# Optimization experiments

Measured on AMD Instinct MI355X. Metric: run time of the kernel, lower is better.

The kernel has to match this reference:

```python
import jax, jax.numpy as jnp
import numpy as np

N_NODES = 40000
N_EDGES = 640000
IN_CH = 128
HID_CH = 128
BN_EPS = 1e-5


def setup_inputs() -> dict:
    key = jax.random.key(0)
    k_x, k_ei, k_w, k_g = jax.random.split(key, 4)
    x = jax.random.normal(k_x, (N_NODES, IN_CH), dtype=jnp.float32)
    edge_index = jax.random.randint(k_ei, (2, N_EDGES), 0, N_NODES, dtype=jnp.int32)
    # Glorot init for GCNConv weight, zero bias (PyG defaults)
    limit = float(np.sqrt(6.0 / (IN_CH + HID_CH)))
    W = jax.random.uniform(k_w, (IN_CH, HID_CH), dtype=jnp.float32, minval=-limit, maxval=limit)
    b = jnp.zeros((HID_CH,), dtype=jnp.float32)
    gamma = jnp.ones((HID_CH,), dtype=jnp.float32)
    beta = jnp.zeros((HID_CH,), dtype=jnp.float32)
    return {"x": x, "edge_index": edge_index, "W": W, "b": b, "gamma": gamma, "beta": beta}


def reference(x, edge_index, W, b, gamma, beta):
    N = x.shape[0]
    src, dst = edge_index[0], edge_index[1]

    # --- GCNConv: h = x @ W, symmetric-normalized aggregation with self-loops ---
    h = x @ W  # [N, H]
    ones = jnp.ones((src.shape[0],), dtype=x.dtype)
    deg = jax.ops.segment_sum(ones, dst, num_segments=N) + 1.0  # +1 for self-loop
    dinv = jax.lax.rsqrt(deg)  # deg >= 1 always
    norm = dinv[src] * dinv[dst]  # [E]
    msg = h[src] * norm[:, None]  # [E, H] gather
    agg = jax.ops.segment_sum(msg, dst, num_segments=N)  # scatter-add
    agg = agg + h * (dinv * dinv)[:, None]  # self-loop contribution
    out = agg + b  # bias added after aggregation (PyG GCNConv)

    # --- BatchNorm1d (training mode: batch stats, biased variance) ---
    mean = jnp.mean(out, axis=0)
    var = jnp.mean((out - mean) ** 2, axis=0)
    out = gamma * (out - mean) * jax.lax.rsqrt(var + BN_EPS) + beta

    # --- ReLU (dropout is a no-op in eval) ---
    return jax.nn.relu(out)
```

## Files before the change

kernel.cpp:

```cpp
#include <hip/hip_runtime.h>

#define N_NODES 40000
#define N_EDGES 640000
#define CH 128
#define BN_EPS 1e-5f
#define CAP 48
#define CNT_S 8
#define MM_ROWS 32
#define MM_BLOCKS (N_NODES / MM_ROWS)
#define FILL_BLOCKS (N_EDGES / 512)


typedef __bf16 bf16x8 __attribute__((ext_vector_type(8)));
typedef float f32x4 __attribute__((ext_vector_type(4)));

__device__ __forceinline__ float bf_lo(unsigned u) { return __uint_as_float(u << 16); }
__device__ __forceinline__ float bf_hi(unsigned u) { return __uint_as_float(u & 0xffff0000u); }
__device__ __forceinline__ unsigned short f2bf(float f) {
    unsigned u = __float_as_uint(f);
    unsigned r = 0x7fffu + ((u >> 16) & 1u);
    return (unsigned short)((u + r) >> 16);
}
__device__ __forceinline__ unsigned pack2bf(float a, float b) {
    return (unsigned)f2bf(a) | ((unsigned)f2bf(b) << 16);
}

__global__ __launch_bounds__(256) void mm_kernel(const float* __restrict__ x,
                                                 const float* __restrict__ W,
                                                 unsigned short* __restrict__ hbf) {
    __shared__ unsigned xl[MM_ROWS * 68];
    int t = threadIdx.x;
    int bb = blockIdx.x;
    size_t row0 = (size_t)bb * MM_ROWS;
#pragma unroll
    for (int it = 0; it < MM_ROWS * 32 / 256; ++it) {
        int idx = it * 256 + t;
        int row = idx >> 5, c4 = idx & 31;
        float4 f = ((const float4*)(x + (row0 + row) * CH))[c4];
        uint2 p;
        p.x = pack2bf(f.x, f.y);
        p.y = pack2bf(f.z, f.w);
        *(uint2*)&xl[row * 68 + 2 * c4] = p;
    }
    int w = t >> 6, l = t & 63;
    int q = l >> 4, c15 = l & 15;
    int ct0 = 2 * w, ct1 = 2 * w + 1;
    bf16x8 bf0[4], bf1[4];
#pragma unroll
    for (int ks = 0; ks < 4; ++ks) {
        const float* wp = W + (size_t)(ks * 32 + 8 * q) * CH + c15;
        float v0[8], v1[8];
#pragma unroll
        for (int j = 0; j < 8; ++j) {
            v0[j] = wp[j * CH + ct0 * 16];
            v1[j] = wp[j * CH + ct1 * 16];
        }
        uint4 u0, u1;
        u0.x = pack2bf(v0[0], v0[1]); u0.y = pack2bf(v0[2], v0[3]);
        u0.z = pack2bf(v0[4], v0[5]); u0.w = pack2bf(v0[6], v0[7]);
        u1.x = pack2bf(v1[0], v1[1]); u1.y = pack2bf(v1[2], v1[3]);
        u1.z = pack2bf(v1[4], v1[5]); u1.w = pack2bf(v1[6], v1[7]);
        bf0[ks] = __builtin_bit_cast(bf16x8, u0);
        bf1[ks] = __builtin_bit_cast(bf16x8, u1);
    }
    __syncthreads();
#pragma unroll
    for (int rt = 0; rt < MM_ROWS / 16; ++rt) {
        int rbase = rt * 16 + c15;
        f32x4 acc0 = {0.f, 0.f, 0.f, 0.f};
        f32x4 acc1 = {0.f, 0.f, 0.f, 0.f};
#pragma unroll
        for (int ks = 0; ks < 4; ++ks) {
            uint4 ua = *(const uint4*)&xl[rbase * 68 + ks * 16 + 4 * q];
            bf16x8 af = __builtin_bit_cast(bf16x8, ua);
            acc0 = __builtin_amdgcn_mfma_f32_16x16x32_bf16(af, bf0[ks], acc0, 0, 0, 0);
            acc1 = __builtin_amdgcn_mfma_f32_16x16x32_bf16(af, bf1[ks], acc1, 0, 0, 0);
        }
        unsigned short* hr = hbf + (row0 + rt * 16 + q * 4) * CH;
#pragma unroll
        for (int r = 0; r < 4; ++r) {
            hr[r * CH + ct0 * 16 + c15] = f2bf(acc0[r]);
            hr[r * CH + ct1 * 16 + c15] = f2bf(acc1[r]);
        }
    }
}

__global__ __launch_bounds__(256) void fill_kernel(const int* __restrict__ src,
                                                   const int* __restrict__ dst,
                                                   int* __restrict__ cnt,
                                                   unsigned short* __restrict__ bucket16) {
    int t = threadIdx.x;
    int bb = blockIdx.x;
    int base = cnt[N_NODES * CNT_S];
    int i0 = bb * 512 + t;
    int i1 = i0 + 256;
    int d0 = dst[i0], d1 = dst[i1];
    int s0 = src[i0], s1 = src[i1];
    int sl0 = atomicAdd(&cnt[d0 * CNT_S], 1) - base;
    int sl1 = atomicAdd(&cnt[d1 * CNT_S], 1) - base;
    if (sl0 < CAP) bucket16[d0 * CAP + sl0] = (unsigned short)s0;
    if (sl1 < CAP) bucket16[d1 * CAP + sl1] = (unsigned short)s1;
}

__global__ __launch_bounds__(256) void aggregate_kernel(const unsigned short* __restrict__ bucket16,
                                                        const int* __restrict__ cnt,
                                                        const unsigned short* __restrict__ hbf,
                                                        const float* __restrict__ b,
                                                        float* __restrict__ out,
                                                        float* __restrict__ sums32) {
    __shared__ float bsum[CH], bsq[CH];
    int t = threadIdx.x;
    if (t < CH) { bsum[t] = 0.0f; bsq[t] = 0.0f; }
    __syncthreads();
    int base = cnt[N_NODES * CNT_S];
    int wid = t >> 6;
    int lane = t & 63;
    int quarter = lane >> 4;
    int ql = lane & 15;
    const uint4* h4 = (const uint4*)hbf;
    float4 bv0 = ((const float4*)b)[ql * 2];
    float4 bv1 = ((const float4*)b)[ql * 2 + 1];
    int n_base = blockIdx.x * 16 + wid * 4;
    float s0 = 0, s1 = 0, s2 = 0, s3 = 0, s4 = 0, s5 = 0, s6 = 0, s7 = 0;
    float q0 = 0, q1 = 0, q2 = 0, q3 = 0, q4 = 0, q5 = 0, q6 = 0, q7 = 0;
#pragma unroll 1
    for (int it = 0; it < 4; ++it) {
        int n = n_base + it;
        int cn = cnt[n * CNT_S] - base;
        int m = cn < CAP ? cn : CAP;
        float dn = rsqrtf((float)cn + 1.0f);
        unsigned sx_pre = (lane < m) ? (unsigned)bucket16[n * CAP + lane] : 0u;
        float a0 = 0, a1 = 0, a2 = 0, a3 = 0, a4 = 0, a5 = 0, a6 = 0, a7 = 0;
        for (int jj = 0; jj < m; jj += 16) {
            int e = jj + quarter * 4;
            unsigned sx0 = (unsigned)__shfl((int)sx_pre, e, 64);
            unsigned sx1 = (unsigned)__shfl((int)sx_pre, e + 1, 64);
            unsigned sx2 = (unsigned)__shfl((int)sx_pre, e + 2, 64);
            unsigned sx3 = (unsigned)__shfl((int)sx_pre, e + 3, 64);
            int c0g = cnt[sx0 * CNT_S];
            int c1g = cnt[sx1 * CNT_S];
            int c2g = cnt[sx2 * CNT_S];
            int c3g = cnt[sx3 * CNT_S];
            uint4 r0 = h4[(size_t)sx0 * 16 + ql];
            uint4 r1 = h4[(size_t)sx1 * 16 + ql];
            uint4 r2 = h4[(size_t)sx2 * 16 + ql];
            uint4 r3 = h4[(size_t)sx3 * 16 + ql];
            float d0 = (e     < m) ? rsqrtf((float)(c0g - base) + 1.0f) : 0.0f;
            float d1 = (e + 1 < m) ? rsqrtf((float)(c1g - base) + 1.0f) : 0.0f;
            float d2 = (e + 2 < m) ? rsqrtf((float)(c2g - base) + 1.0f) : 0.0f;
            float d3 = (e + 3 < m) ? rsqrtf((float)(c3g - base) + 1.0f) : 0.0f;
            a0 += bf_lo(r0.x) * d0; a1 += bf_hi(r0.x) * d0;
            a2 += bf_lo(r0.y) * d0; a3 += bf_hi(r0.y) * d0;
            a4 += bf_lo(r0.z) * d0; a5 += bf_hi(r0.z) * d0;
            a6 += bf_lo(r0.w) * d0; a7 += bf_hi(r0.w) * d0;
            a0 += bf_lo(r1.x) * d1; a1 += bf_hi(r1.x) * d1;
            a2 += bf_lo(r1.y) * d1; a3 += bf_hi(r1.y) * d1;
            a4 += bf_lo(r1.z) * d1; a5 += bf_hi(r1.z) * d1;
            a6 += bf_lo(r1.w) * d1; a7 += bf_hi(r1.w) * d1;
            a0 += bf_lo(r2.x) * d2; a1 += bf_hi(r2.x) * d2;
            a2 += bf_lo(r2.y) * d2; a3 += bf_hi(r2.y) * d2;
            a4 += bf_lo(r2.z) * d2; a5 += bf_hi(r2.z) * d2;
            a6 += bf_lo(r2.w) * d2; a7 += bf_hi(r2.w) * d2;
            a0 += bf_lo(r3.x) * d3; a1 += bf_hi(r3.x) * d3;
            a2 += bf_lo(r3.y) * d3; a3 += bf_hi(r3.y) * d3;
            a4 += bf_lo(r3.z) * d3; a5 += bf_hi(r3.z) * d3;
            a6 += bf_lo(r3.w) * d3; a7 += bf_hi(r3.w) * d3;
        }
        a0 += __shfl_xor(a0, 16, 64); a0 += __shfl_xor(a0, 32, 64);
        a1 += __shfl_xor(a1, 16, 64); a1 += __shfl_xor(a1, 32, 64);
        a2 += __shfl_xor(a2, 16, 64); a2 += __shfl_xor(a2, 32, 64);
        a3 += __shfl_xor(a3, 16, 64); a3 += __shfl_xor(a3, 32, 64);
        a4 += __shfl_xor(a4, 16, 64); a4 += __shfl_xor(a4, 32, 64);
        a5 += __shfl_xor(a5, 16, 64); a5 += __shfl_xor(a5, 32, 64);
        a6 += __shfl_xor(a6, 16, 64); a6 += __shfl_xor(a6, 32, 64);
        a7 += __shfl_xor(a7, 16, 64); a7 += __shfl_xor(a7, 32, 64);
        if (quarter == 0) {
            uint4 raw = h4[(size_t)n * 16 + ql];
            float sq = dn * dn;
            float o0 = a0 * dn + bf_lo(raw.x) * sq + bv0.x;
            float o1 = a1 * dn + bf_hi(raw.x) * sq + bv0.y;
            float o2 = a2 * dn + bf_lo(raw.y) * sq + bv0.z;
            float o3 = a3 * dn + bf_hi(raw.y) * sq + bv0.w;
            float o4 = a4 * dn + bf_lo(raw.z) * sq + bv1.x;
            float o5 = a5 * dn + bf_hi(raw.z) * sq + bv1.y;
            float o6 = a6 * dn + bf_lo(raw.w) * sq + bv1.z;
            float o7 = a7 * dn + bf_hi(raw.w) * sq + bv1.w;
            float4* op = (float4*)(out + (size_t)n * CH + ql * 8);
            float4 w0 = {o0, o1, o2, o3};
            float4 w1 = {o4, o5, o6, o7};
            op[0] = w0;
            op[1] = w1;
            s0 += o0; q0 += o0 * o0;
            s1 += o1; q1 += o1 * o1;
            s2 += o2; q2 += o2 * o2;
            s3 += o3; q3 += o3 * o3;
            s4 += o4; q4 += o4 * o4;
            s5 += o5; q5 += o5 * o5;
            s6 += o6; q6 += o6 * o6;
            s7 += o7; q7 += o7 * o7;
        }
    }
    if (quarter == 0) {
        int c0 = ql * 8;
        atomicAdd(&bsum[c0 + 0], s0); atomicAdd(&bsq[c0 + 0], q0);
        atomicAdd(&bsum[c0 + 1], s1); atomicAdd(&bsq[c0 + 1], q1);
        atomicAdd(&bsum[c0 + 2], s2); atomicAdd(&bsq[c0 + 2], q2);
        atomicAdd(&bsum[c0 + 3], s3); atomicAdd(&bsq[c0 + 3], q3);
        atomicAdd(&bsum[c0 + 4], s4); atomicAdd(&bsq[c0 + 4], q4);
        atomicAdd(&bsum[c0 + 5], s5); atomicAdd(&bsq[c0 + 5], q5);
        atomicAdd(&bsum[c0 + 6], s6); atomicAdd(&bsq[c0 + 6], q6);
        atomicAdd(&bsum[c0 + 7], s7); atomicAdd(&bsq[c0 + 7], q7);
    }
    __syncthreads();
    atomicAdd(&sums32[(blockIdx.x & 31) * 256 + t], (t < CH) ? bsum[t] : bsq[t - CH]);
}

__global__ __launch_bounds__(256) void bn_relu_kernel(float* __restrict__ out,
                                                      const float* __restrict__ sums32,
                                                      const float* __restrict__ gamma,
                                                      const float* __restrict__ beta) {
    __shared__ float sc[CH], sh[CH];
    int t = threadIdx.x;
    if (t < CH) {
        float P = sums32[32 * 256];
        float s = -32.0f * P, q = -32.0f * P;
#pragma unroll
        for (int k = 0; k < 32; ++k) {
            s += sums32[k * 256 + t];
            q += sums32[k * 256 + CH + t];
        }
        const float invN = 1.0f / (float)N_NODES;
        float mean = s * invN;
        float var = q * invN - mean * mean;
        float scale = gamma[t] * rsqrtf(var + BN_EPS);
        sc[t] = scale;
        sh[t] = beta[t] - mean * scale;
    }
    __syncthreads();
    int i = blockIdx.x * 256 + t;
    int c0 = (i & 31) * 4;
    float4 v = ((float4*)out)[i];
    float r0 = v.x * sc[c0] + sh[c0];
    float r1 = v.y * sc[c0 + 1] + sh[c0 + 1];
    float r2 = v.z * sc[c0 + 2] + sh[c0 + 2];
    float r3 = v.w * sc[c0 + 3] + sh[c0 + 3];
    v.x = r0 > 0.0f ? r0 : 0.0f;
    v.y = r1 > 0.0f ? r1 : 0.0f;
    v.z = r2 > 0.0f ? r2 : 0.0f;
    v.w = r3 > 0.0f ? r3 : 0.0f;
    ((float4*)out)[i] = v;
}

extern "C" void kernel_launch(void* const* d_in, const int* in_sizes, int n_in,
                              void* d_out, int out_size, void* d_ws, size_t ws_size,
                              hipStream_t stream) {
    const float* x = (const float*)d_in[0];
    const int* ei = (const int*)d_in[1];
    const float* W = (const float*)d_in[2];
    const float* b = (const float*)d_in[3];
    const float* gamma = (const float*)d_in[4];
    const float* beta = (const float*)d_in[5];
    float* out = (float*)d_out;
    const int* src = ei;
    const int* dst = ei + N_EDGES;
    char* ws = (char*)d_ws;

    unsigned short* hbf = (unsigned short*)ws;
    int* cnt = (int*)(ws + 10240000);
    float* sums32 = (float*)(ws + 11520256);
    unsigned short* bucket16 = (unsigned short*)(ws + 11553280);

    mm_kernel<<<MM_BLOCKS, 256, 0, stream>>>(x, W, hbf);
    fill_kernel<<<FILL_BLOCKS, 256, 0, stream>>>(src, dst, cnt, bucket16);
    aggregate_kernel<<<N_NODES / 16, 256, 0, stream>>>(bucket16, cnt, hbf, b, out, sums32);
    bn_relu_kernel<<<N_NODES * CH / 4 / 256, 256, 0, stream>>>(out, sums32, gamma, beta);
}
```

Before: 167.2 us.

## Prescale h by source dinv in matmul and simplify gather with zero row

Reorders the kernels so the edge fill runs before the matmul. The matmul then multiplies each output row by its node's dinv, which removes the per-edge degree lookup and rsqrt from the aggregation. The aggregation now has each lane own two channels and issue sixteen independent 4-byte row gathers per step, with masked slots pointing at an appended zero row instead of using predicated weights. The self-loop term comes for free because the node's own prescaled row is added before the final dinv multiply. The trade-offs are narrower per-lane loads and a slightly larger workspace.

```diff
diff --git a/kernel.cpp b/kernel.cpp
--- a/kernel.cpp
+++ b/kernel.cpp
@@ -9,6 +9,7 @@
 #define MM_ROWS 32
 #define MM_BLOCKS (N_NODES / MM_ROWS)
 #define FILL_BLOCKS (N_EDGES / 512)
+#define ZROW 40000
 
 
 typedef __bf16 bf16x8 __attribute__((ext_vector_type(8)));
@@ -25,72 +26,14 @@
     return (unsigned)f2bf(a) | ((unsigned)f2bf(b) << 16);
 }
 
-__global__ __launch_bounds__(256) void mm_kernel(const float* __restrict__ x,
-                                                 const float* __restrict__ W,
-                                                 unsigned short* __restrict__ hbf) {
-    __shared__ unsigned xl[MM_ROWS * 68];
-    int t = threadIdx.x;
-    int bb = blockIdx.x;
-    size_t row0 = (size_t)bb * MM_ROWS;
-#pragma unroll
-    for (int it = 0; it < MM_ROWS * 32 / 256; ++it) {
-        int idx = it * 256 + t;
-        int row = idx >> 5, c4 = idx & 31;
-        float4 f = ((const float4*)(x + (row0 + row) * CH))[c4];
-        uint2 p;
-        p.x = pack2bf(f.x, f.y);
-        p.y = pack2bf(f.z, f.w);
-        *(uint2*)&xl[row * 68 + 2 * c4] = p;
-    }
-    int w = t >> 6, l = t & 63;
-    int q = l >> 4, c15 = l & 15;
-    int ct0 = 2 * w, ct1 = 2 * w + 1;
-    bf16x8 bf0[4], bf1[4];
-#pragma unroll
-    for (int ks = 0; ks < 4; ++ks) {
-        const float* wp = W + (size_t)(ks * 32 + 8 * q) * CH + c15;
-        float v0[8], v1[8];
-#pragma unroll
-        for (int j = 0; j < 8; ++j) {
-            v0[j] = wp[j * CH + ct0 * 16];
-            v1[j] = wp[j * CH + ct1 * 16];
-        }
-        uint4 u0, u1;
-        u0.x = pack2bf(v0[0], v0[1]); u0.y = pack2bf(v0[2], v0[3]);
-        u0.z = pack2bf(v0[4], v0[5]); u0.w = pack2bf(v0[6], v0[7]);
-        u1.x = pack2bf(v1[0], v1[1]); u1.y = pack2bf(v1[2], v1[3]);
-        u1.z = pack2bf(v1[4], v1[5]); u1.w = pack2bf(v1[6], v1[7]);
-        bf0[ks] = __builtin_bit_cast(bf16x8, u0);
-        bf1[ks] = __builtin_bit_cast(bf16x8, u1);
-    }
-    __syncthreads();
-#pragma unroll
-    for (int rt = 0; rt < MM_ROWS / 16; ++rt) {
-        int rbase = rt * 16 + c15;
-        f32x4 acc0 = {0.f, 0.f, 0.f, 0.f};
-        f32x4 acc1 = {0.f, 0.f, 0.f, 0.f};
-#pragma unroll
-        for (int ks = 0; ks < 4; ++ks) {
-            uint4 ua = *(const uint4*)&xl[rbase * 68 + ks * 16 + 4 * q];
-            bf16x8 af = __builtin_bit_cast(bf16x8, ua);
-            acc0 = __builtin_amdgcn_mfma_f32_16x16x32_bf16(af, bf0[ks], acc0, 0, 0, 0);
-            acc1 = __builtin_amdgcn_mfma_f32_16x16x32_bf16(af, bf1[ks], acc1, 0, 0, 0);
-        }
-        unsigned short* hr = hbf + (row0 + rt * 16 + q * 4) * CH;
-#pragma unroll
-        for (int r = 0; r < 4; ++r) {
-            hr[r * CH + ct0 * 16 + c15] = f2bf(acc0[r]);
-            hr[r * CH + ct1 * 16 + c15] = f2bf(acc1[r]);
-        }
-    }
-}
-
 __global__ __launch_bounds__(256) void fill_kernel(const int* __restrict__ src,
                                                    const int* __restrict__ dst,
                                                    int* __restrict__ cnt,
-                                                   unsigned short* __restrict__ bucket16) {
+                                                   unsigned short* __restrict__ bucket16,
+                                                   unsigned* __restrict__ hbf_u32) {
     int t = threadIdx.x;
     int bb = blockIdx.x;
+    if (bb == 0 && t < 64) hbf_u32[(size_t)ZROW * 64 + t] = 0u;
     int base = cnt[N_NODES * CNT_S];
     int i0 = bb * 512 + t;
     int i1 = i0 + 256;
@@ -102,9 +45,77 @@
     if (sl1 < CAP) bucket16[d1 * CAP + sl1] = (unsigned short)s1;
 }
 
+__global__ __launch_bounds__(256) void mm_kernel(const float* __restrict__ x,
+                                                 const float* __restrict__ W,
+                                                 const int* __restrict__ cnt,
+                                                 unsigned short* __restrict__ hbf) {
+    __shared__ unsigned xl[MM_ROWS * 68];
+    __shared__ float dinv_l[MM_ROWS];
+    int t = threadIdx.x;
+    int bb = blockIdx.x;
+    size_t row0 = (size_t)bb * MM_ROWS;
+    if (t < MM_ROWS) {
+        int base = cnt[N_NODES * CNT_S];
+        int c = cnt[(row0 + t) * CNT_S] - base;
+        dinv_l[t] = rsqrtf((float)c + 1.0f);
+    }
+#pragma unroll
+    for (int it = 0; it < MM_ROWS * 32 / 256; ++it) {
+        int idx = it * 256 + t;
+        int row = idx >> 5, c4 = idx & 31;
+        float4 f = ((const float4*)(x + (row0 + row) * CH))[c4];
+        uint2 p;
+        p.x = pack2bf(f.x, f.y);
+        p.y = pack2bf(f.z, f.w);
+        *(uint2*)&xl[row * 68 + 2 * c4] = p;
+    }
+    int w = t >> 6, l = t & 63;
+    int q = l >> 4, c15 = l & 15;
+    int ct0 = 2 * w, ct1 = 2 * w + 1;
+    bf16x8 bf0[4], bf1[4];
+#pragma unroll
+    for (int ks = 0; ks < 4; ++ks) {
+        const float* wp = W + (size_t)(ks * 32 + 8 * q) * CH + c15;
+        float v0[8], v1[8];
+#pragma unroll
+        for (int j = 0; j < 8; ++j) {
+            v0[j] = wp[j * CH + ct0 * 16];
+            v1[j] = wp[j * CH + ct1 * 16];
+        }
+        uint4 u0, u1;
+        u0.x = pack2bf(v0[0], v0[1]); u0.y = pack2bf(v0[2], v0[3]);
+        u0.z = pack2bf(v0[4], v0[5]); u0.w = pack2bf(v0[6], v0[7]);
+        u1.x = pack2bf(v1[0], v1[1]); u1.y = pack2bf(v1[2], v1[3]);
+        u1.z = pack2bf(v1[4], v1[5]); u1.w = pack2bf(v1[6], v1[7]);
+        bf0[ks] = __builtin_bit_cast(bf16x8, u0);
+        bf1[ks] = __builtin_bit_cast(bf16x8, u1);
+    }
+    __syncthreads();
+#pragma unroll
+    for (int rt = 0; rt < MM_ROWS / 16; ++rt) {
+        int rbase = rt * 16 + c15;
+        f32x4 acc0 = {0.f, 0.f, 0.f, 0.f};
+        f32x4 acc1 = {0.f, 0.f, 0.f, 0.f};
+#pragma unroll
+        for (int ks = 0; ks < 4; ++ks) {
+            uint4 ua = *(const uint4*)&xl[rbase * 68 + ks * 16 + 4 * q];
+            bf16x8 af = __builtin_bit_cast(bf16x8, ua);
+            acc0 = __builtin_amdgcn_mfma_f32_16x16x32_bf16(af, bf0[ks], acc0, 0, 0, 0);
+            acc1 = __builtin_amdgcn_mfma_f32_16x16x32_bf16(af, bf1[ks], acc1, 0, 0, 0);
+        }
+        unsigned short* hr = hbf + (row0 + rt * 16 + q * 4) * CH;
+#pragma unroll
+        for (int r = 0; r < 4; ++r) {
+            float dv = dinv_l[rt * 16 + q * 4 + r];
+            hr[r * CH + ct0 * 16 + c15] = f2bf(acc0[r] * dv);
+            hr[r * CH + ct1 * 16 + c15] = f2bf(acc1[r] * dv);
+        }
+    }
+}
+
 __global__ __launch_bounds__(256) void aggregate_kernel(const unsigned short* __restrict__ bucket16,
                                                         const int* __restrict__ cnt,
-                                                        const unsigned short* __restrict__ hbf,
+                                                        const unsigned* __restrict__ hbf_u32,
                                                         const float* __restrict__ b,
                                                         float* __restrict__ out,
                                                         float* __restrict__ sums32) {
@@ -115,102 +126,51 @@
     int base = cnt[N_NODES * CNT_S];
     int wid = t >> 6;
     int lane = t & 63;
-    int quarter = lane >> 4;
-    int ql = lane & 15;
-    const uint4* h4 = (const uint4*)hbf;
-    float4 bv0 = ((const float4*)b)[ql * 2];
-    float4 bv1 = ((const float4*)b)[ql * 2 + 1];
     int n_base = blockIdx.x * 16 + wid * 4;
-    float s0 = 0, s1 = 0, s2 = 0, s3 = 0, s4 = 0, s5 = 0, s6 = 0, s7 = 0;
-    float q0 = 0, q1 = 0, q2 = 0, q3 = 0, q4 = 0, q5 = 0, q6 = 0, q7 = 0;
-#pragma unroll 1
+    float2 bv = ((const float2*)b)[lane];
+
+    int cn[4];
+    unsigned bp[4], us[4];
+#pragma unroll
+    for (int it = 0; it < 4; ++it) cn[it] = cnt[(n_base + it) * CNT_S] - base;
+#pragma unroll
+    for (int it = 0; it < 4; ++it) bp[it] = (unsigned)bucket16[(n_base + it) * CAP + lane];
+#pragma unroll
+    for (int it = 0; it < 4; ++it) us[it] = hbf_u32[(size_t)(n_base + it) * 64 + lane];
+
+    float slo = 0.f, shi = 0.f, qlo = 0.f, qhi = 0.f;
+#pragma unroll
     for (int it = 0; it < 4; ++it) {
         int n = n_base + it;
-        int cn = cnt[n * CNT_S] - base;
-        int m = cn < CAP ? cn : CAP;
-        float dn = rsqrtf((float)cn + 1.0f);
-        unsigned sx_pre = (lane < m) ? (unsigned)bucket16[n * CAP + lane] : 0u;
-        float a0 = 0, a1 = 0, a2 = 0, a3 = 0, a4 = 0, a5 = 0, a6 = 0, a7 = 0;
+        int m = cn[it] < CAP ? cn[it] : CAP;
+        float dn = rsqrtf((float)cn[it] + 1.0f);
+        unsigned sp = (lane < m) ? bp[it] : (unsigned)ZROW;
+        float alo = bf_lo(us[it]);
+        float ahi = bf_hi(us[it]);
         for (int jj = 0; jj < m; jj += 16) {
-            int e = jj + quarter * 4;
-            unsigned sx0 = (unsigned)__shfl((int)sx_pre, e, 64);
-            unsigned sx1 = (unsigned)__shfl((int)sx_pre, e + 1, 64);
-            unsigned sx2 = (unsigned)__shfl((int)sx_pre, e + 2, 64);
-            unsigned sx3 = (unsigned)__shfl((int)sx_pre, e + 3, 64);
-            int c0g = cnt[sx0 * CNT_S];
-            int c1g = cnt[sx1 * CNT_S];
-            int c2g = cnt[sx2 * CNT_S];
-            int c3g = cnt[sx3 * CNT_S];
-            uint4 r0 = h4[(size_t)sx0 * 16 + ql];
-            uint4 r1 = h4[(size_t)sx1 * 16 + ql];
-            uint4 r2 = h4[(size_t)sx2 * 16 + ql];
-            uint4 r3 = h4[(size_t)sx3 * 16 + ql];
-            float d0 = (e     < m) ? rsqrtf((float)(c0g - base) + 1.0f) : 0.0f;
-            float d1 = (e + 1 < m) ? rsqrtf((float)(c1g - base) + 1.0f) : 0.0f;
-            float d2 = (e + 2 < m) ? rsqrtf((float)(c2g - base) + 1.0f) : 0.0f;
-            float d3 = (e + 3 < m) ? rsqrtf((float)(c3g - base) + 1.0f) : 0.0f;
-            a0 += bf_lo(r0.x) * d0; a1 += bf_hi(r0.x) * d0;
-            a2 += bf_lo(r0.y) * d0; a3 += bf_hi(r0.y) * d0;
-            a4 += bf_lo(r0.z) * d0; a5 += bf_hi(r0.z) * d0;
-            a6 += bf_lo(r0.w) * d0; a7 += bf_hi(r0.w) * d0;
-            a0 += bf_lo(r1.x) * d1; a1 += bf_hi(r1.x) * d1;
-            a2 += bf_lo(r1.y) * d1; a3 += bf_hi(r1.y) * d1;
-            a4 += bf_lo(r1.z) * d1; a5 += bf_hi(r1.z) * d1;
-            a6 += bf_lo(r1.w) * d1; a7 += bf_hi(r1.w) * d1;
-            a0 += bf_lo(r2.x) * d2; a1 += bf_hi(r2.x) * d2;
-            a2 += bf_lo(r2.y) * d2; a3 += bf_hi(r2.y) * d2;
-            a4 += bf_lo(r2.z) * d2; a5 += bf_hi(r2.z) * d2;
-            a6 += bf_lo(r2.w) * d2; a7 += bf_hi(r2.w) * d2;
-            a0 += bf_lo(r3.x) * d3; a1 += bf_hi(r3.x) * d3;
-            a2 += bf_lo(r3.y) * d3; a3 += bf_hi(r3.y) * d3;
-            a4 += bf_lo(r3.z) * d3; a5 += bf_hi(r3.z) * d3;
-            a6 += bf_lo(r3.w) * d3; a7 += bf_hi(r3.w) * d3;
-        }
-        a0 += __shfl_xor(a0, 16, 64); a0 += __shfl_xor(a0, 32, 64);
-        a1 += __shfl_xor(a1, 16, 64); a1 += __shfl_xor(a1, 32, 64);
-        a2 += __shfl_xor(a2, 16, 64); a2 += __shfl_xor(a2, 32, 64);
-        a3 += __shfl_xor(a3, 16, 64); a3 += __shfl_xor(a3, 32, 64);
-        a4 += __shfl_xor(a4, 16, 64); a4 += __shfl_xor(a4, 32, 64);
-        a5 += __shfl_xor(a5, 16, 64); a5 += __shfl_xor(a5, 32, 64);
-        a6 += __shfl_xor(a6, 16, 64); a6 += __shfl_xor(a6, 32, 64);
-        a7 += __shfl_xor(a7, 16, 64); a7 += __shfl_xor(a7, 32, 64);
-        if (quarter == 0) {
-            uint4 raw = h4[(size_t)n * 16 + ql];
-            float sq = dn * dn;
-            float o0 = a0 * dn + bf_lo(raw.x) * sq + bv0.x;
-            float o1 = a1 * dn + bf_hi(raw.x) * sq + bv0.y;
-            float o2 = a2 * dn + bf_lo(raw.y) * sq + bv0.z;
-            float o3 = a3 * dn + bf_hi(raw.y) * sq + bv0.w;
-            float o4 = a4 * dn + bf_lo(raw.z) * sq + bv1.x;
-            float o5 = a5 * dn + bf_hi(raw.z) * sq + bv1.y;
-            float o6 = a6 * dn + bf_lo(raw.w) * sq + bv1.z;
-            float o7 = a7 * dn + bf_hi(raw.w) * sq + bv1.w;
-            float4* op = (float4*)(out + (size_t)n * CH + ql * 8);
-            float4 w0 = {o0, o1, o2, o3};
-            float4 w1 = {o4, o5, o6, o7};
-            op[0] = w0;
-            op[1] = w1;
-            s0 += o0; q0 += o0 * o0;
-            s1 += o1; q1 += o1 * o1;
-            s2 += o2; q2 += o2 * o2;
-            s3 += o3; q3 += o3 * o3;
-            s4 += o4; q4 += o4 * o4;
-            s5 += o5; q5 += o5 * o5;
-            s6 += o6; q6 += o6 * o6;
-            s7 += o7; q7 += o7 * o7;
-        }
-    }
-    if (quarter == 0) {
-        int c0 = ql * 8;
-        atomicAdd(&bsum[c0 + 0], s0); atomicAdd(&bsq[c0 + 0], q0);
-        atomicAdd(&bsum[c0 + 1], s1); atomicAdd(&bsq[c0 + 1], q1);
-        atomicAdd(&bsum[c0 + 2], s2); atomicAdd(&bsq[c0 + 2], q2);
-        atomicAdd(&bsum[c0 + 3], s3); atomicAdd(&bsq[c0 + 3], q3);
-        atomicAdd(&bsum[c0 + 4], s4); atomicAdd(&bsq[c0 + 4], q4);
-        atomicAdd(&bsum[c0 + 5], s5); atomicAdd(&bsq[c0 + 5], q5);
-        atomicAdd(&bsum[c0 + 6], s6); atomicAdd(&bsq[c0 + 6], q6);
-        atomicAdd(&bsum[c0 + 7], s7); atomicAdd(&bsq[c0 + 7], q7);
-    }
+            unsigned u[16];
+#pragma unroll
+            for (int r = 0; r < 16; ++r) {
+                unsigned sx = (unsigned)__shfl((int)sp, jj + r, 64);
+                u[r] = hbf_u32[(size_t)sx * 64 + lane];
+            }
+#pragma unroll
+            for (int r = 0; r < 16; ++r) {
+                alo += bf_lo(u[r]);
+                ahi += bf_hi(u[r]);
+            }
+        }
+        float olo = alo * dn + bv.x;
+        float ohi = ahi * dn + bv.y;
+        float2 ov = {olo, ohi};
+        *(float2*)(out + (size_t)n * CH + 2 * lane) = ov;
+        slo += olo; qlo += olo * olo;
+        shi += ohi; qhi += ohi * ohi;
+    }
+    atomicAdd(&bsum[2 * lane], slo);
+    atomicAdd(&bsum[2 * lane + 1], shi);
+    atomicAdd(&bsq[2 * lane], qlo);
+    atomicAdd(&bsq[2 * lane + 1], qhi);
     __syncthreads();
     atomicAdd(&sums32[(blockIdx.x & 31) * 256 + t], (t < CH) ? bsum[t] : bsq[t - CH]);
 }
@@ -266,12 +226,13 @@
     char* ws = (char*)d_ws;
 
     unsigned short* hbf = (unsigned short*)ws;
-    int* cnt = (int*)(ws + 10240000);
-    float* sums32 = (float*)(ws + 11520256);
-    unsigned short* bucket16 = (unsigned short*)(ws + 11553280);
-
-    mm_kernel<<<MM_BLOCKS, 256, 0, stream>>>(x, W, hbf);
-    fill_kernel<<<FILL_BLOCKS, 256, 0, stream>>>(src, dst, cnt, bucket16);
-    aggregate_kernel<<<N_NODES / 16, 256, 0, stream>>>(bucket16, cnt, hbf, b, out, sums32);
+    int* cnt = (int*)(ws + 10240256);
+    float* sums32 = (float*)(ws + 11520512);
+    unsigned short* bucket16 = (unsigned short*)(ws + 11553536);
+
+    fill_kernel<<<FILL_BLOCKS, 256, 0, stream>>>(src, dst, cnt, bucket16, (unsigned*)hbf);
+    mm_kernel<<<MM_BLOCKS, 256, 0, stream>>>(x, W, cnt, hbf);
+    aggregate_kernel<<<N_NODES / 16, 256, 0, stream>>>(bucket16, cnt, (const unsigned*)hbf,
+                                                       b, out, sums32);
     bn_relu_kernel<<<N_NODES * CH / 4 / 256, 256, 0, stream>>>(out, sums32, gamma, beta);
 }
```

Measured after the change: 161.9 us. 1.03x faster.
